# Kernel tuning notes

Measured on AMD Instinct MI355X. Metric: run time of the kernel, lower is better.

## Reference

```python
import jax, jax.numpy as jnp
import numpy as np

H, D = 12, 768
DH = D // H  # 64

def setup_inputs() -> dict:
    key = jax.random.key(0)
    ks = jax.random.split(key, 9)
    s = 0.02
    x  = jax.random.normal(ks[0], (8, 1024, D), dtype=jnp.float32)
    Wq = jax.random.normal(ks[1], (H, D, DH), dtype=jnp.float32) * s
    Wk = jax.random.normal(ks[2], (H, D, DH), dtype=jnp.float32) * s
    Wv = jax.random.normal(ks[3], (H, D, DH), dtype=jnp.float32) * s
    bq = jax.random.normal(ks[4], (H, DH), dtype=jnp.float32) * s
    bk = jax.random.normal(ks[5], (H, DH), dtype=jnp.float32) * s
    bv = jax.random.normal(ks[6], (H, DH), dtype=jnp.float32) * s
    Wo = jax.random.normal(ks[7], (D, D), dtype=jnp.float32) * s
    bo = jax.random.normal(ks[8], (D,), dtype=jnp.float32) * s
    return {"x": x, "Wq": Wq, "Wk": Wk, "Wv": Wv, "bq": bq, "bk": bk, "bv": bv, "Wo": Wo, "bo": bo}

def reference(x, Wq, Wk, Wv, bq, bk, bv, Wo, bo):
    # x: [B,S,D]; per-head projections batched over heads: [B,H,S,DH]
    q = jnp.einsum('bsd,hde->bhse', x, Wq) + bq[None, :, None, :]
    k = jnp.einsum('bsd,hde->bhse', x, Wk) + bk[None, :, None, :]
    v = jnp.einsum('bsd,hde->bhse', x, Wv) + bv[None, :, None, :]
    scores = jnp.einsum('bhse,bhte->bhst', q, k) / jnp.sqrt(jnp.float32(DH))
    probs = jax.nn.softmax(scores, axis=-1)  # dropout is identity (p=0 / eval)
    ctx = jnp.einsum('bhst,bhte->bhse', probs, v)  # [B,H,S,DH]
    B, _, S, _ = ctx.shape
    # concat heads along feature dim (head order matches torch cat order)
    ctx = jnp.transpose(ctx, (0, 2, 1, 3)).reshape(B, S, H * DH)
    out = jnp.einsum('bsd,de->bse', ctx, Wo) + bo
    return out
```

## Files before the change

kernel.cpp:

```cpp
#include <hip/hip_runtime.h>
#include <math.h>


constexpr int NB  = 8;
constexpr int SEQ = 1024;
constexpr int NH  = 12;
constexpr int DM  = 768;
constexpr int DHD = 64;
constexpr int MROWS = NB * SEQ;
constexpr int NQKV  = 3 * NH * DHD;

typedef __attribute__((ext_vector_type(8))) short short8;
typedef __attribute__((ext_vector_type(4))) float f32x4;

#define MFMA16(a,b,c) __builtin_amdgcn_mfma_f32_16x16x32_bf16((a),(b),(c),0,0,0)

#if __has_builtin(__builtin_amdgcn_exp2f)
#define EXP2(x) __builtin_amdgcn_exp2f(x)
#else
#define EXP2(x) exp2f(x)
#endif

__device__ __forceinline__ unsigned short f2bf(float f) {
    unsigned u = __float_as_uint(f);
    return (unsigned short)((u + 0x7fffu + ((u >> 16) & 1u)) >> 16);
}
__device__ __forceinline__ unsigned short f2bf_fast(float f) {
    return (unsigned short)((__float_as_uint(f) + 0x8000u) >> 16);
}

__device__ __forceinline__ void gl_lds16(const unsigned short* g, unsigned short* l) {
    __builtin_amdgcn_global_load_lds(
        (const __attribute__((address_space(1))) void*)g,
        (__attribute__((address_space(3))) void*)l, 16, 0, 0);
}

__device__ __forceinline__ void stageA(unsigned short* lds, const unsigned short* gbase,
                                       int i, int ln, int ldg) {
    int r    = i * 16 + (ln >> 2);
    int cpos = ln & 3;
    int cdat = (cpos - (r >> 1)) & 3;
    gl_lds16(gbase + (size_t)r * ldg + cdat * 8, lds + i * 512);
}
__device__ __forceinline__ short8 ldA(const unsigned short* buf, int row, int quad) {
    int c = (quad + (row >> 1)) & 3;
    return *(const short8*)&buf[row * 32 + c * 8];
}

__device__ __forceinline__ void stageK(unsigned short* lds, const unsigned short* gbase,
                                       int i, int ln, int ldg) {
    int r    = i * 8 + (ln >> 3);
    int cpos = ln & 7;
    int cdat = (cpos - r) & 7;
    gl_lds16(gbase + (size_t)r * ldg + cdat * 8, lds + i * 512);
}
__device__ __forceinline__ short8 ldK(const unsigned short* buf, int row, int chunk) {
    int c = (chunk + row) & 7;
    return *(const short8*)&buf[row * 64 + c * 8];
}

__global__ __launch_bounds__(256) void cvtx_k(const float* __restrict__ x,
                                              unsigned short* __restrict__ xb, int n4) {
    int i = blockIdx.x * 256 + threadIdx.x;
    if (i >= n4) return;
    float4 v = ((const float4*)x)[i];
    ushort4 o;
    o.x = f2bf(v.x); o.y = f2bf(v.y); o.z = f2bf(v.z); o.w = f2bf(v.w);
    ((ushort4*)xb)[i] = o;
}

__global__ __launch_bounds__(256) void wt_k(const float* __restrict__ W,
                                            unsigned short* __restrict__ t,
                                            int R, int C, size_t sIn, size_t sOut) {
    __shared__ float tb[64][65];
    const int bz = blockIdx.z;
    W += (size_t)bz * sIn;
    t += (size_t)bz * sOut;
    const int r0 = blockIdx.x * 64, c0 = blockIdx.y * 64;
    const int tid = threadIdx.x;
    const int rr = tid >> 2, cc = (tid & 3) * 16;
#pragma unroll
    for (int j = 0; j < 16; j += 4) {
        float4 v = *(const float4*)&W[(size_t)(r0 + rr) * C + c0 + cc + j];
        tb[rr][cc + j + 0] = v.x;
        tb[rr][cc + j + 1] = v.y;
        tb[rr][cc + j + 2] = v.z;
        tb[rr][cc + j + 3] = v.w;
    }
    __syncthreads();
#pragma unroll
    for (int j = 0; j < 16; ++j)
        t[(size_t)(c0 + rr) * R + r0 + cc + j] = f2bf(tb[cc + j][rr]);
}

__global__ __launch_bounds__(256, 3) void qkv_mfma_k(
    const unsigned short* __restrict__ xb, const unsigned short* __restrict__ wt,
    const float* __restrict__ bq, const float* __restrict__ bk, const float* __restrict__ bv,
    unsigned short* __restrict__ qb, unsigned short* __restrict__ kb,
    unsigned short* __restrict__ vT) {
    __shared__ unsigned short Ah[128 * 32], Bh[128 * 32];

    const int tid = threadIdx.x;
    const int wv = tid >> 6, ln = tid & 63, quad = ln >> 4, lnid = ln & 15;
    const int row0 = blockIdx.x * 128, col0 = blockIdx.y * 128;

    f32x4 acc[2][8];
#pragma unroll
    for (int i = 0; i < 2; ++i)
#pragma unroll
        for (int j = 0; j < 8; ++j) acc[i][j] = (f32x4){0.f, 0.f, 0.f, 0.f};

    const unsigned short* Ahg = xb + (size_t)row0 * DM;
    const unsigned short* Bhg = wt + (size_t)col0 * DM;

    for (int kc = 0; kc < DM; kc += 32) {
        __syncthreads();
        stageA(Ah, Ahg + kc, wv * 2, ln, DM);
        stageA(Ah, Ahg + kc, wv * 2 + 1, ln, DM);
        stageA(Bh, Bhg + kc, wv * 2, ln, DM);
        stageA(Bh, Bhg + kc, wv * 2 + 1, ln, DM);
        __syncthreads();

        short8 ah0 = ldA(Ah, wv * 32 + lnid, quad);
        short8 ah1 = ldA(Ah, wv * 32 + 16 + lnid, quad);
#pragma unroll
        for (int nt = 0; nt < 8; ++nt) {
            short8 b_h = ldA(Bh, nt * 16 + lnid, quad);
            acc[0][nt] = MFMA16(ah0, b_h, acc[0][nt]);
            acc[1][nt] = MFMA16(ah1, b_h, acc[1][nt]);
        }
    }

    const int sel = col0 / DM;
    const float scale = (sel == 0) ? 0.18033688011112042f : 1.0f;
    const float* bias = (sel == 0) ? bq : (sel == 1 ? bk : bv);
    unsigned short* oh = (sel == 0) ? qb : kb;

#pragma unroll
    for (int mt = 0; mt < 2; ++mt) {
#pragma unroll
        for (int nt = 0; nt < 8; ++nt) {
            const int e_glob = col0 + nt * 16 + lnid;
            const int he = e_glob - sel * DM;
            const int hh2 = he >> 6, ee = he & 63;
            const float bs = bias[he];
            if (sel < 2) {
#pragma unroll
                for (int r = 0; r < 4; ++r) {
                    const int srow = row0 + wv * 32 + mt * 16 + quad * 4 + r;
                    const int bb = srow >> 10, ss = srow & (SEQ - 1);
                    oh[((size_t)(bb * NH + hh2) * SEQ + ss) * DHD + ee] =
                        f2bf((acc[mt][nt][r] + bs) * scale);
                }
            } else {
                const int srow = row0 + wv * 32 + mt * 16 + quad * 4;
                const int bb = srow >> 10, ss = srow & (SEQ - 1);
                ushort4 pk;
                pk.x = f2bf(acc[mt][nt][0] + bs);
                pk.y = f2bf(acc[mt][nt][1] + bs);
                pk.z = f2bf(acc[mt][nt][2] + bs);
                pk.w = f2bf(acc[mt][nt][3] + bs);
                *(ushort4*)&vT[((size_t)(bb * NH + hh2) * DHD + ee) * SEQ + ss] = pk;
            }
        }
    }
}

__global__ __launch_bounds__(256, 3) void attn_mfma_k(
    const unsigned short* __restrict__ qb, const unsigned short* __restrict__ kb,
    const unsigned short* __restrict__ vT, unsigned short* __restrict__ ctb) {
    __shared__ unsigned short ksh[64 * 64], vsm[64 * 64];
    __shared__ unsigned short ps[128 * 72];

    const int tid = threadIdx.x;
    const int wv = tid >> 6, ln = tid & 63, quad = ln >> 4, lnid = ln & 15;
    const int bhid = blockIdx.x % 96, qt = blockIdx.x / 96;
    const int b = bhid / NH, h = bhid % NH;
    const int q0 = qt * 128;
    const size_t bh = (size_t)bhid;
    const unsigned short* qhb = qb + bh * (SEQ * DHD);
    const unsigned short* khb = kb + bh * (SEQ * DHD);
    const unsigned short* vTb = vT + bh * (DHD * SEQ);

    short8 qf[2][2];
#pragma unroll
    for (int mt = 0; mt < 2; ++mt) {
        const int srow = q0 + wv * 32 + mt * 16 + lnid;
#pragma unroll
        for (int ks_ = 0; ks_ < 2; ++ks_)
            qf[mt][ks_] = *(const short8*)(qhb + (size_t)srow * DHD + ks_ * 32 + quad * 8);
    }

    f32x4 ctx[2][4];
#pragma unroll
    for (int i = 0; i < 2; ++i)
#pragma unroll
        for (int j = 0; j < 4; ++j) ctx[i][j] = (f32x4){0.f, 0.f, 0.f, 0.f};
    float lsum[2][4] = {};

    for (int kt = 0; kt < SEQ / 64; ++kt) {
        __syncthreads();
        stageK(ksh, khb + kt * 64 * DHD, wv * 2, ln, DHD);
        stageK(ksh, khb + kt * 64 * DHD, wv * 2 + 1, ln, DHD);
        stageK(vsm, vTb + kt * 64, wv * 2, ln, SEQ);
        stageK(vsm, vTb + kt * 64, wv * 2 + 1, ln, SEQ);
        __syncthreads();

        f32x4 sc[2][4];
#pragma unroll
        for (int i = 0; i < 2; ++i)
#pragma unroll
            for (int j = 0; j < 4; ++j) sc[i][j] = (f32x4){0.f, 0.f, 0.f, 0.f};
#pragma unroll
        for (int ks_ = 0; ks_ < 2; ++ks_) {
#pragma unroll
            for (int nt = 0; nt < 4; ++nt) {
                short8 k_h = ldK(ksh, nt * 16 + lnid, ks_ * 4 + quad);
                sc[0][nt] = MFMA16(qf[0][ks_], k_h, sc[0][nt]);
                sc[1][nt] = MFMA16(qf[1][ks_], k_h, sc[1][nt]);
            }
        }

#pragma unroll
        for (int mt = 0; mt < 2; ++mt)
#pragma unroll
            for (int nt = 0; nt < 4; ++nt)
#pragma unroll
                for (int r = 0; r < 4; ++r) {
                    float p = EXP2(sc[mt][nt][r]);
                    lsum[mt][r] += p;
                    ps[(wv * 32 + mt * 16 + quad * 4 + r) * 72 + nt * 16 + lnid] =
                        f2bf_fast(p);
                }

#pragma unroll
        for (int kvs = 0; kvs < 2; ++kvs) {
            short8 pa0 = *(const short8*)&ps[(wv * 32 + lnid) * 72 + kvs * 32 + quad * 8];
            short8 pa1 = *(const short8*)&ps[(wv * 32 + 16 + lnid) * 72 + kvs * 32 + quad * 8];
#pragma unroll
            for (int nt = 0; nt < 4; ++nt) {
                short8 v8 = ldK(vsm, nt * 16 + lnid, kvs * 4 + quad);
                ctx[0][nt] = MFMA16(pa0, v8, ctx[0][nt]);
                ctx[1][nt] = MFMA16(pa1, v8, ctx[1][nt]);
            }
        }
    }

#pragma unroll
    for (int mt = 0; mt < 2; ++mt) {
#pragma unroll
        for (int r = 0; r < 4; ++r) {
            float s = lsum[mt][r];
#pragma unroll
            for (int off = 1; off < 16; off <<= 1) s += __shfl_xor(s, off, 64);
            const float inv = 1.0f / s;
            const int srow = b * SEQ + q0 + wv * 32 + mt * 16 + quad * 4 + r;
#pragma unroll
            for (int nt = 0; nt < 4; ++nt)
                ctb[(size_t)srow * DM + h * DHD + nt * 16 + lnid] =
                    f2bf(ctx[mt][nt][r] * inv);
        }
    }
}

__global__ __launch_bounds__(256, 4) void out_mfma_k(
    const unsigned short* __restrict__ ctb, const unsigned short* __restrict__ wot,
    const float* __restrict__ bo, float* __restrict__ out) {
    __shared__ unsigned short Ah[128 * 32], Bh[64 * 32];

    const int tid = threadIdx.x;
    const int wv = tid >> 6, ln = tid & 63, quad = ln >> 4, lnid = ln & 15;
    const int row0 = blockIdx.x * 128, col0 = blockIdx.y * 64;

    f32x4 acc[2][4];
#pragma unroll
    for (int i = 0; i < 2; ++i)
#pragma unroll
        for (int j = 0; j < 4; ++j) acc[i][j] = (f32x4){0.f, 0.f, 0.f, 0.f};

    const unsigned short* Ahg = ctb + (size_t)row0 * DM;
    const unsigned short* Bhg = wot + (size_t)col0 * DM;

    for (int kc = 0; kc < DM; kc += 32) {
        __syncthreads();
        stageA(Ah, Ahg + kc, wv * 2, ln, DM);
        stageA(Ah, Ahg + kc, wv * 2 + 1, ln, DM);
        stageA(Bh, Bhg + kc, wv, ln, DM);
        __syncthreads();

        short8 ah0 = ldA(Ah, wv * 32 + lnid, quad);
        short8 ah1 = ldA(Ah, wv * 32 + 16 + lnid, quad);
#pragma unroll
        for (int nt = 0; nt < 4; ++nt) {
            short8 b_h = ldA(Bh, nt * 16 + lnid, quad);
            acc[0][nt] = MFMA16(ah0, b_h, acc[0][nt]);
            acc[1][nt] = MFMA16(ah1, b_h, acc[1][nt]);
        }
    }

#pragma unroll
    for (int mt = 0; mt < 2; ++mt)
#pragma unroll
        for (int nt = 0; nt < 4; ++nt) {
            const int col = col0 + nt * 16 + lnid;
            const float bs = bo[col];
#pragma unroll
            for (int r = 0; r < 4; ++r) {
                const int srow = row0 + wv * 32 + mt * 16 + quad * 4 + r;
                out[(size_t)srow * DM + col] = acc[mt][nt][r] + bs;
            }
        }
}

extern "C" void kernel_launch(void* const* d_in, const int* in_sizes, int n_in,
                              void* d_out, int out_size, void* d_ws, size_t ws_size,
                              hipStream_t stream) {
    const float* x  = (const float*)d_in[0];
    const float* Wq = (const float*)d_in[1];
    const float* Wk = (const float*)d_in[2];
    const float* Wv = (const float*)d_in[3];
    const float* bq = (const float*)d_in[4];
    const float* bk = (const float*)d_in[5];
    const float* bv = (const float*)d_in[6];
    const float* Wo = (const float*)d_in[7];
    const float* bo = (const float*)d_in[8];
    float* out = (float*)d_out;

    char* w = (char*)d_ws;
    const size_t elsX = (size_t)MROWS * DM;
    const size_t elsQ = (size_t)NB * NH * SEQ * DHD;
    unsigned short* xb  = (unsigned short*)w;
    unsigned short* ctb = xb;
    size_t off = elsX * 2;
    unsigned short* wt  = (unsigned short*)(w + off); off += (size_t)NQKV * DM * 2;
    unsigned short* wot = (unsigned short*)(w + off); off += (size_t)DM * DM * 2;
    unsigned short* qbp = (unsigned short*)(w + off); off += elsQ * 2;
    unsigned short* kbp = (unsigned short*)(w + off); off += elsQ * 2;
    unsigned short* vTp = (unsigned short*)(w + off); off += elsQ * 2;

    cvtx_k<<<dim3((int)(elsX / 4 / 256)), 256, 0, stream>>>(x, xb, (int)(elsX / 4));
    const size_t whsz = (size_t)DM * DHD;
    wt_k<<<dim3(12, 1, 12), 256, 0, stream>>>(Wq, wt + 0 * 12 * whsz, DM, DHD, whsz, whsz);
    wt_k<<<dim3(12, 1, 12), 256, 0, stream>>>(Wk, wt + 1 * 12 * whsz, DM, DHD, whsz, whsz);
    wt_k<<<dim3(12, 1, 12), 256, 0, stream>>>(Wv, wt + 2 * 12 * whsz, DM, DHD, whsz, whsz);
    wt_k<<<dim3(12, 12, 1), 256, 0, stream>>>(Wo, wot, DM, DM, 0, 0);

    qkv_mfma_k<<<dim3(MROWS / 128, NQKV / 128), 256, 0, stream>>>(
        xb, wt, bq, bk, bv, qbp, kbp, vTp);
    attn_mfma_k<<<dim3(768), 256, 0, stream>>>(qbp, kbp, vTp, ctb);
    out_mfma_k<<<dim3(MROWS / 128, DM / 64), 256, 0, stream>>>(ctb, wot, bo, out);
}
```

Before: 211.1 us.

## Fuse prep kernels, use 2x2 wave tiling in GEMMs, double-buffer attention K/V

Merges the x-conversion kernel and the four weight-transpose kernels into one launch. The QKV and output GEMMs switch to a 2x2 wave layout with 4x4 MFMA tiles per wave, and the output GEMM tile grows to 128x128, so each wave reuses more fragments loaded from LDS. The attention kernel double-buffers its K/V LDS tiles, loading the next tile while the current one is computed, which removes one barrier per iteration. The cost is more LDS and registers, which may lower occupancy, and fewer blocks in the output GEMM.

```diff
diff --git a/kernel.cpp b/kernel.cpp
--- a/kernel.cpp
+++ b/kernel.cpp
@@ -59,25 +59,37 @@
     return *(const short8*)&buf[row * 64 + c * 8];
 }
 
-__global__ __launch_bounds__(256) void cvtx_k(const float* __restrict__ x,
-                                              unsigned short* __restrict__ xb, int n4) {
-    int i = blockIdx.x * 256 + threadIdx.x;
-    if (i >= n4) return;
-    float4 v = ((const float4*)x)[i];
-    ushort4 o;
-    o.x = f2bf(v.x); o.y = f2bf(v.y); o.z = f2bf(v.z); o.w = f2bf(v.w);
-    ((ushort4*)xb)[i] = o;
-}
-
-__global__ __launch_bounds__(256) void wt_k(const float* __restrict__ W,
-                                            unsigned short* __restrict__ t,
-                                            int R, int C, size_t sIn, size_t sOut) {
+__global__ __launch_bounds__(256) void prep_k(
+    const float* __restrict__ x,
+    const float* __restrict__ Wq, const float* __restrict__ Wk,
+    const float* __restrict__ Wv, const float* __restrict__ Wo,
+    unsigned short* __restrict__ xb, unsigned short* __restrict__ wt,
+    unsigned short* __restrict__ wot) {
     __shared__ float tb[64][65];
-    const int bz = blockIdx.z;
-    W += (size_t)bz * sIn;
-    t += (size_t)bz * sOut;
-    const int r0 = blockIdx.x * 64, c0 = blockIdx.y * 64;
-    const int tid = threadIdx.x;
+    const int blk = blockIdx.x, tid = threadIdx.x;
+    if (blk < 6144) {
+        const int i = blk * 256 + tid;
+        float4 v = ((const float4*)x)[i];
+        ushort4 o;
+        o.x = f2bf(v.x); o.y = f2bf(v.y); o.z = f2bf(v.z); o.w = f2bf(v.w);
+        ((ushort4*)xb)[i] = o;
+        return;
+    }
+    const int t = blk - 6144;
+    const int job = t / 144, lb = t % 144;
+    const float* W;
+    unsigned short* dst;
+    int C, r0, c0;
+    if (job < 3) {
+        const float* Ws = (job == 0) ? Wq : (job == 1 ? Wk : Wv);
+        const int h = lb / 12, rb = lb % 12;
+        W = Ws + (size_t)h * (DM * DHD);
+        dst = wt + (size_t)(job * 12 + h) * (DM * DHD);
+        C = DHD; r0 = rb * 64; c0 = 0;
+    } else {
+        W = Wo; dst = wot; C = DM;
+        r0 = (lb / 12) * 64; c0 = (lb % 12) * 64;
+    }
     const int rr = tid >> 2, cc = (tid & 3) * 16;
 #pragma unroll
     for (int j = 0; j < 16; j += 4) {
@@ -90,7 +102,7 @@
     __syncthreads();
 #pragma unroll
     for (int j = 0; j < 16; ++j)
-        t[(size_t)(c0 + rr) * R + r0 + cc + j] = f2bf(tb[cc + j][rr]);
+        dst[(size_t)(c0 + rr) * DM + r0 + cc + j] = f2bf(tb[cc + j][rr]);
 }
 
 __global__ __launch_bounds__(256, 3) void qkv_mfma_k(
@@ -102,13 +114,14 @@
 
     const int tid = threadIdx.x;
     const int wv = tid >> 6, ln = tid & 63, quad = ln >> 4, lnid = ln & 15;
+    const int wvm = wv >> 1, wvn = wv & 1;
     const int row0 = blockIdx.x * 128, col0 = blockIdx.y * 128;
 
-    f32x4 acc[2][8];
-#pragma unroll
-    for (int i = 0; i < 2; ++i)
-#pragma unroll
-        for (int j = 0; j < 8; ++j) acc[i][j] = (f32x4){0.f, 0.f, 0.f, 0.f};
+    f32x4 acc[4][4];
+#pragma unroll
+    for (int i = 0; i < 4; ++i)
+#pragma unroll
+        for (int j = 0; j < 4; ++j) acc[i][j] = (f32x4){0.f, 0.f, 0.f, 0.f};
 
     const unsigned short* Ahg = xb + (size_t)row0 * DM;
     const unsigned short* Bhg = wt + (size_t)col0 * DM;
@@ -121,45 +134,46 @@
         stageA(Bh, Bhg + kc, wv * 2 + 1, ln, DM);
         __syncthreads();
 
-        short8 ah0 = ldA(Ah, wv * 32 + lnid, quad);
-        short8 ah1 = ldA(Ah, wv * 32 + 16 + lnid, quad);
-#pragma unroll
-        for (int nt = 0; nt < 8; ++nt) {
-            short8 b_h = ldA(Bh, nt * 16 + lnid, quad);
-            acc[0][nt] = MFMA16(ah0, b_h, acc[0][nt]);
-            acc[1][nt] = MFMA16(ah1, b_h, acc[1][nt]);
-        }
-    }
-
-    const int sel = col0 / DM;
+        short8 a[4], b[4];
+#pragma unroll
+        for (int i = 0; i < 4; ++i) a[i] = ldA(Ah, wvm * 64 + i * 16 + lnid, quad);
+#pragma unroll
+        for (int j = 0; j < 4; ++j) b[j] = ldA(Bh, wvn * 64 + j * 16 + lnid, quad);
+#pragma unroll
+        for (int i = 0; i < 4; ++i)
+#pragma unroll
+            for (int j = 0; j < 4; ++j) acc[i][j] = MFMA16(a[i], b[j], acc[i][j]);
+    }
+
+    const int sel = (col0 >= 2 * DM) ? 2 : (col0 >= DM ? 1 : 0);
     const float scale = (sel == 0) ? 0.18033688011112042f : 1.0f;
     const float* bias = (sel == 0) ? bq : (sel == 1 ? bk : bv);
     unsigned short* oh = (sel == 0) ? qb : kb;
 
 #pragma unroll
-    for (int mt = 0; mt < 2; ++mt) {
-#pragma unroll
-        for (int nt = 0; nt < 8; ++nt) {
-            const int e_glob = col0 + nt * 16 + lnid;
-            const int he = e_glob - sel * DM;
+    for (int i = 0; i < 4; ++i) {
+#pragma unroll
+        for (int j = 0; j < 4; ++j) {
+            const int col = col0 + wvn * 64 + j * 16 + lnid;
+            const int he = col - sel * DM;
             const int hh2 = he >> 6, ee = he & 63;
             const float bs = bias[he];
             if (sel < 2) {
 #pragma unroll
                 for (int r = 0; r < 4; ++r) {
-                    const int srow = row0 + wv * 32 + mt * 16 + quad * 4 + r;
+                    const int srow = row0 + wvm * 64 + i * 16 + quad * 4 + r;
                     const int bb = srow >> 10, ss = srow & (SEQ - 1);
                     oh[((size_t)(bb * NH + hh2) * SEQ + ss) * DHD + ee] =
-                        f2bf((acc[mt][nt][r] + bs) * scale);
+                        f2bf((acc[i][j][r] + bs) * scale);
                 }
             } else {
-                const int srow = row0 + wv * 32 + mt * 16 + quad * 4;
+                const int srow = row0 + wvm * 64 + i * 16 + quad * 4;
                 const int bb = srow >> 10, ss = srow & (SEQ - 1);
                 ushort4 pk;
-                pk.x = f2bf(acc[mt][nt][0] + bs);
-                pk.y = f2bf(acc[mt][nt][1] + bs);
-                pk.z = f2bf(acc[mt][nt][2] + bs);
-                pk.w = f2bf(acc[mt][nt][3] + bs);
+                pk.x = f2bf(acc[i][j][0] + bs);
+                pk.y = f2bf(acc[i][j][1] + bs);
+                pk.z = f2bf(acc[i][j][2] + bs);
+                pk.w = f2bf(acc[i][j][3] + bs);
                 *(ushort4*)&vT[((size_t)(bb * NH + hh2) * DHD + ee) * SEQ + ss] = pk;
             }
         }
@@ -169,7 +183,7 @@
 __global__ __launch_bounds__(256, 3) void attn_mfma_k(
     const unsigned short* __restrict__ qb, const unsigned short* __restrict__ kb,
     const unsigned short* __restrict__ vT, unsigned short* __restrict__ ctb) {
-    __shared__ unsigned short ksh[64 * 64], vsm[64 * 64];
+    __shared__ unsigned short ksh[2][64 * 64], vsm[2][64 * 64];
     __shared__ unsigned short ps[128 * 72];
 
     const int tid = threadIdx.x;
@@ -177,10 +191,9 @@
     const int bhid = blockIdx.x % 96, qt = blockIdx.x / 96;
     const int b = bhid / NH, h = bhid % NH;
     const int q0 = qt * 128;
-    const size_t bh = (size_t)bhid;
-    const unsigned short* qhb = qb + bh * (SEQ * DHD);
-    const unsigned short* khb = kb + bh * (SEQ * DHD);
-    const unsigned short* vTb = vT + bh * (DHD * SEQ);
+    const unsigned short* qhb = qb + (size_t)bhid * (SEQ * DHD);
+    const unsigned short* khb = kb + (size_t)bhid * (SEQ * DHD);
+    const unsigned short* vTb = vT + (size_t)bhid * (DHD * SEQ);
 
     short8 qf[2][2];
 #pragma unroll
@@ -198,13 +211,22 @@
         for (int j = 0; j < 4; ++j) ctx[i][j] = (f32x4){0.f, 0.f, 0.f, 0.f};
     float lsum[2][4] = {};
 
+    stageK(ksh[0], khb, wv * 2, ln, DHD);
+    stageK(ksh[0], khb, wv * 2 + 1, ln, DHD);
+    stageK(vsm[0], vTb, wv * 2, ln, SEQ);
+    stageK(vsm[0], vTb, wv * 2 + 1, ln, SEQ);
+
     for (int kt = 0; kt < SEQ / 64; ++kt) {
-        __syncthreads();
-        stageK(ksh, khb + kt * 64 * DHD, wv * 2, ln, DHD);
-        stageK(ksh, khb + kt * 64 * DHD, wv * 2 + 1, ln, DHD);
-        stageK(vsm, vTb + kt * 64, wv * 2, ln, SEQ);
-        stageK(vsm, vTb + kt * 64, wv * 2 + 1, ln, SEQ);
-        __syncthreads();
+        const int cur = kt & 1;
+        __syncthreads();
+        if (kt + 1 < SEQ / 64) {
+            const unsigned short* kn = khb + (kt + 1) * 64 * DHD;
+            const unsigned short* vn = vTb + (kt + 1) * 64;
+            stageK(ksh[cur ^ 1], kn, wv * 2, ln, DHD);
+            stageK(ksh[cur ^ 1], kn, wv * 2 + 1, ln, DHD);
+            stageK(vsm[cur ^ 1], vn, wv * 2, ln, SEQ);
+            stageK(vsm[cur ^ 1], vn, wv * 2 + 1, ln, SEQ);
+        }
 
         f32x4 sc[2][4];
 #pragma unroll
@@ -215,7 +237,7 @@
         for (int ks_ = 0; ks_ < 2; ++ks_) {
 #pragma unroll
             for (int nt = 0; nt < 4; ++nt) {
-                short8 k_h = ldK(ksh, nt * 16 + lnid, ks_ * 4 + quad);
+                short8 k_h = ldK(ksh[cur], nt * 16 + lnid, ks_ * 4 + quad);
                 sc[0][nt] = MFMA16(qf[0][ks_], k_h, sc[0][nt]);
                 sc[1][nt] = MFMA16(qf[1][ks_], k_h, sc[1][nt]);
             }
@@ -239,7 +261,7 @@
             short8 pa1 = *(const short8*)&ps[(wv * 32 + 16 + lnid) * 72 + kvs * 32 + quad * 8];
 #pragma unroll
             for (int nt = 0; nt < 4; ++nt) {
-                short8 v8 = ldK(vsm, nt * 16 + lnid, kvs * 4 + quad);
+                short8 v8 = ldK(vsm[cur], nt * 16 + lnid, kvs * 4 + quad);
                 ctx[0][nt] = MFMA16(pa0, v8, ctx[0][nt]);
                 ctx[1][nt] = MFMA16(pa1, v8, ctx[1][nt]);
             }
@@ -263,18 +285,19 @@
     }
 }
 
-__global__ __launch_bounds__(256, 4) void out_mfma_k(
+__global__ __launch_bounds__(256, 3) void out_mfma_k(
     const unsigned short* __restrict__ ctb, const unsigned short* __restrict__ wot,
     const float* __restrict__ bo, float* __restrict__ out) {
-    __shared__ unsigned short Ah[128 * 32], Bh[64 * 32];
+    __shared__ unsigned short Ah[128 * 32], Bh[128 * 32];
 
     const int tid = threadIdx.x;
     const int wv = tid >> 6, ln = tid & 63, quad = ln >> 4, lnid = ln & 15;
-    const int row0 = blockIdx.x * 128, col0 = blockIdx.y * 64;
-
-    f32x4 acc[2][4];
-#pragma unroll
-    for (int i = 0; i < 2; ++i)
+    const int wvm = wv >> 1, wvn = wv & 1;
+    const int row0 = blockIdx.x * 128, col0 = blockIdx.y * 128;
+
+    f32x4 acc[4][4];
+#pragma unroll
+    for (int i = 0; i < 4; ++i)
 #pragma unroll
         for (int j = 0; j < 4; ++j) acc[i][j] = (f32x4){0.f, 0.f, 0.f, 0.f};
 
@@ -285,29 +308,31 @@
         __syncthreads();
         stageA(Ah, Ahg + kc, wv * 2, ln, DM);
         stageA(Ah, Ahg + kc, wv * 2 + 1, ln, DM);
-        stageA(Bh, Bhg + kc, wv, ln, DM);
-        __syncthreads();
-
-        short8 ah0 = ldA(Ah, wv * 32 + lnid, quad);
-        short8 ah1 = ldA(Ah, wv * 32 + 16 + lnid, quad);
-#pragma unroll
-        for (int nt = 0; nt < 4; ++nt) {
-            short8 b_h = ldA(Bh, nt * 16 + lnid, quad);
-            acc[0][nt] = MFMA16(ah0, b_h, acc[0][nt]);
-            acc[1][nt] = MFMA16(ah1, b_h, acc[1][nt]);
-        }
-    }
-
-#pragma unroll
-    for (int mt = 0; mt < 2; ++mt)
-#pragma unroll
-        for (int nt = 0; nt < 4; ++nt) {
-            const int col = col0 + nt * 16 + lnid;
+        stageA(Bh, Bhg + kc, wv * 2, ln, DM);
+        stageA(Bh, Bhg + kc, wv * 2 + 1, ln, DM);
+        __syncthreads();
+
+        short8 a[4], b[4];
+#pragma unroll
+        for (int i = 0; i < 4; ++i) a[i] = ldA(Ah, wvm * 64 + i * 16 + lnid, quad);
+#pragma unroll
+        for (int j = 0; j < 4; ++j) b[j] = ldA(Bh, wvn * 64 + j * 16 + lnid, quad);
+#pragma unroll
+        for (int i = 0; i < 4; ++i)
+#pragma unroll
+            for (int j = 0; j < 4; ++j) acc[i][j] = MFMA16(a[i], b[j], acc[i][j]);
+    }
+
+#pragma unroll
+    for (int i = 0; i < 4; ++i)
+#pragma unroll
+        for (int j = 0; j < 4; ++j) {
+            const int col = col0 + wvn * 64 + j * 16 + lnid;
             const float bs = bo[col];
 #pragma unroll
             for (int r = 0; r < 4; ++r) {
-                const int srow = row0 + wv * 32 + mt * 16 + quad * 4 + r;
-                out[(size_t)srow * DM + col] = acc[mt][nt][r] + bs;
+                const int srow = row0 + wvm * 64 + i * 16 + quad * 4 + r;
+                out[(size_t)srow * DM + col] = acc[i][j][r] + bs;
             }
         }
 }
@@ -338,15 +363,9 @@
     unsigned short* kbp = (unsigned short*)(w + off); off += elsQ * 2;
     unsigned short* vTp = (unsigned short*)(w + off); off += elsQ * 2;
 
-    cvtx_k<<<dim3((int)(elsX / 4 / 256)), 256, 0, stream>>>(x, xb, (int)(elsX / 4));
-    const size_t whsz = (size_t)DM * DHD;
-    wt_k<<<dim3(12, 1, 12), 256, 0, stream>>>(Wq, wt + 0 * 12 * whsz, DM, DHD, whsz, whsz);
-    wt_k<<<dim3(12, 1, 12), 256, 0, stream>>>(Wk, wt + 1 * 12 * whsz, DM, DHD, whsz, whsz);
-    wt_k<<<dim3(12, 1, 12), 256, 0, stream>>>(Wv, wt + 2 * 12 * whsz, DM, DHD, whsz, whsz);
-    wt_k<<<dim3(12, 12, 1), 256, 0, stream>>>(Wo, wot, DM, DM, 0, 0);
-
+    prep_k<<<dim3(6144 + 576), 256, 0, stream>>>(x, Wq, Wk, Wv, Wo, xb, wt, wot);
     qkv_mfma_k<<<dim3(MROWS / 128, NQKV / 128), 256, 0, stream>>>(
         xb, wt, bq, bk, bv, qbp, kbp, vTp);
     attn_mfma_k<<<dim3(768), 256, 0, stream>>>(qbp, kbp, vTp, ctb);
-    out_mfma_k<<<dim3(MROWS / 128, DM / 64), 256, 0, stream>>>(ctb, wot, bo, out);
-}
+    out_mfma_k<<<dim3(MROWS / 128, DM / 128), 256, 0, stream>>>(ctb, wot, bo, out);
+}
```

Result: faster. 203.5 us (-3.6%).
